# Performance work log

Measured on AMD Instinct MI355X. Metric: run time of the kernel, lower is better.

The kernel has to match this reference:

```python
import jax, jax.numpy as jnp
import numpy as np

N_BINS = 229
OUT_F = 88
MODEL = 128
W_SIZE = 30
WIN = 2 * W_SIZE + 1  # 61


def _window(spec):
    B, T, F = spec.shape
    padded = jnp.pad(spec, ((0, 0), (W_SIZE, W_SIZE), (0, 0)))
    idx = jnp.arange(T)[:, None] + jnp.arange(WIN)[None, :]
    return padded[:, idx, :]


def setup_inputs() -> dict:
    key = jax.random.key(0)
    ks = jax.random.split(key, 12)
    B, T = 4, 1024
    s = 0.05
    return {
        "spec": jax.random.normal(ks[0], (B, T, N_BINS), dtype=jnp.float32),
        # frame_stack: Linear(N_BINS -> OUT_F)
        "W_frame": jax.random.normal(ks[1], (N_BINS, OUT_F), dtype=jnp.float32) * s,
        "b_frame": jnp.zeros((OUT_F,), dtype=jnp.float32),
        # onset attention: Linear(N_BINS + N_BINS -> MODEL), v: Linear(MODEL -> 1, no bias)
        "W_attn_o": jax.random.normal(ks[2], (2 * N_BINS, MODEL), dtype=jnp.float32) * s,
        "b_attn_o": jnp.zeros((MODEL,), dtype=jnp.float32),
        "v_o": jax.random.normal(ks[3], (MODEL,), dtype=jnp.float32) * s,
        # onset linear1: Linear(N_BINS -> OUT_F)
        "W_lin1": jax.random.normal(ks[4], (N_BINS, OUT_F), dtype=jnp.float32) * s,
        "b_lin1": jnp.zeros((OUT_F,), dtype=jnp.float32),
        # combine attention: Linear(2*OUT_F + N_BINS -> MODEL)
        "W_attn_c": jax.random.normal(ks[5], (2 * OUT_F + N_BINS, MODEL), dtype=jnp.float32) * s,
        "b_attn_c": jnp.zeros((MODEL,), dtype=jnp.float32),
        "v_c": jax.random.normal(ks[6], (MODEL,), dtype=jnp.float32) * s,
        # combine linear: Linear(2*OUT_F + N_BINS -> OUT_F)
        "W_linc": jax.random.normal(ks[7], (2 * OUT_F + N_BINS, OUT_F), dtype=jnp.float32) * s,
        "b_linc": jnp.zeros((OUT_F,), dtype=jnp.float32),
    }


def _attend(hidden, win, Wa, ba, v):
    B, T, Wn, F = win.shape
    h = jnp.broadcast_to(hidden[:, :, None, :], (B, T, Wn, hidden.shape[-1]))
    energy = jnp.tanh(jnp.concatenate([h, win], axis=-1) @ Wa + ba)
    scores = energy @ v
    return jax.nn.softmax(scores, axis=-1)


def reference(spec, W_frame, b_frame, W_attn_o, b_attn_o, v_o, W_lin1, b_lin1,
              W_attn_c, b_attn_c, v_c, W_linc, b_linc):
    win = _window(spec)

    feat_pred = spec @ W_frame + b_frame  # [B,T,OUT_F]

    # Onset stack
    a_onset = _attend(spec, win, W_attn_o, b_attn_o, v_o)
    weighted_o = jnp.einsum('btw,btwf->btf', a_onset, win)  # [B,T,N_BINS]
    onset_pred = jax.nn.sigmoid(weighted_o @ W_lin1 + b_lin1)  # [B,T,OUT_F]

    # Combine stack
    x = jnp.concatenate([feat_pred, onset_pred], axis=-1)  # [B,T,2*OUT_F]
    a_frame = _attend(x, win, W_attn_c, b_attn_c, v_c)
    weighted_c = jnp.einsum('btw,btwf->btf', a_frame, win)  # [B,T,N_BINS]
    frame_pred = jax.nn.sigmoid(jnp.concatenate([x, weighted_c], axis=-1) @ W_linc + b_linc)

    return (frame_pred, a_frame[:, :, None, :], onset_pred, a_onset[:, :, None, :], feat_pred)
```

## Files before the change

kernel.cpp:

```cpp
#include <hip/hip_runtime.h>

#define NBINS 229
#define OUTF  88
#define MODEL 128
#define WSZ   30
#define WIN   61
#define TLEN  1024
#define BT    4096

#define NC1 648
#define NP1 704
#define NC2 216

typedef short bf16x8 __attribute__((ext_vector_type(8)));
typedef float f32x4 __attribute__((ext_vector_type(4)));
typedef unsigned short ushort_t;

__device__ __forceinline__ float sigmoid_f(float x) {
    return __builtin_amdgcn_rcpf(1.f + __expf(-x));
}
__device__ __forceinline__ ushort_t f2bf(float f) {
    unsigned u = __float_as_uint(f);
    return (ushort_t)((u + 0x7fffu + ((u >> 16) & 1u)) >> 16);
}

__device__ __forceinline__ float dot8(uint4 pv, float4 ha, float4 hb,
                                      float4 va, float4 vb) {
    float r;
    r  = va.x * __builtin_amdgcn_rcpf(__builtin_fmaf(ha.x, __uint_as_float(pv.x << 16), 1.f));
    r += va.y * __builtin_amdgcn_rcpf(__builtin_fmaf(ha.y, __uint_as_float(pv.x & 0xffff0000u), 1.f));
    r += va.z * __builtin_amdgcn_rcpf(__builtin_fmaf(ha.z, __uint_as_float(pv.y << 16), 1.f));
    r += va.w * __builtin_amdgcn_rcpf(__builtin_fmaf(ha.w, __uint_as_float(pv.y & 0xffff0000u), 1.f));
    r += vb.x * __builtin_amdgcn_rcpf(__builtin_fmaf(hb.x, __uint_as_float(pv.z << 16), 1.f));
    r += vb.y * __builtin_amdgcn_rcpf(__builtin_fmaf(hb.y, __uint_as_float(pv.z & 0xffff0000u), 1.f));
    r += vb.z * __builtin_amdgcn_rcpf(__builtin_fmaf(hb.z, __uint_as_float(pv.w << 16), 1.f));
    r += vb.w * __builtin_amdgcn_rcpf(__builtin_fmaf(hb.w, __uint_as_float(pv.w & 0xffff0000u), 1.f));
    return r;
}

__device__ __forceinline__ bf16x8 cvt8(f32x4 a, f32x4 b) {
    bf16x8 r;
    r[0] = (short)f2bf(a.x); r[1] = (short)f2bf(a.y);
    r[2] = (short)f2bf(a.z); r[3] = (short)f2bf(a.w);
    r[4] = (short)f2bf(b.x); r[5] = (short)f2bf(b.y);
    r[6] = (short)f2bf(b.z); r[7] = (short)f2bf(b.w);
    return r;
}
__device__ __forceinline__ bf16x8 loadA(const float* sp, int k0) {
    if (k0 > 228) return (bf16x8)(short)0;
    f32x4 a, b;
    __builtin_memcpy(&a, sp + k0, 16);
    if (k0 <= 216) {
        __builtin_memcpy(&b, sp + k0 + 4, 16);
    } else {
        b = (f32x4){sp[228], 0.f, 0.f, 0.f};
    }
    return cvt8(a, b);
}

#define GP_BLOCKS 897

__global__ __launch_bounds__(256) void gemm_prep(
    const float* __restrict__ spec,
    const float* __restrict__ Wf,  const float* __restrict__ bfr,
    const float* __restrict__ Wao, const float* __restrict__ bao,
    const float* __restrict__ Wl1,
    const float* __restrict__ Wac, const float* __restrict__ bac,
    const float* __restrict__ Wlc,
    const float* __restrict__ vo,  const float* __restrict__ vc,
    float* __restrict__ feat, float* __restrict__ EHo_,
    ushort_t* __restrict__ EPo_, ushort_t* __restrict__ EPc_,
    ushort_t* __restrict__ Rb_,  ushort_t* __restrict__ Qb_,
    ushort_t* __restrict__ B2b, float* __restrict__ bias2,
    float* __restrict__ sv)
{
    __shared__ ushort_t B1t[64 * 256];
    __shared__ float red[4];
    const int tid = threadIdx.x;
    const int b = blockIdx.x;

    if (b < 704) {
        const int e = b & 7, kf = b >> 3;
        const int rb = (e * 8 + (kf & 7)) * 64;
        const int cb = (kf >> 3) * 64;

        {
            const int n  = tid & 63;
            const int kq = tid >> 6;
            const int ng = cb + n;
            const float* srcp = nullptr; int sstr = 0;
            if (ng < 88)       { srcp = Wf  + ng;                          sstr = 88;  }
            else if (ng < 216) { srcp = Wao + (ng - 88);                   sstr = 128; }
            else if (ng < 344) { srcp = Wao + (size_t)NBINS * 128 + (ng - 216); sstr = 128; }
            else if (ng < 472) { srcp = Wac + (size_t)176 * 128 + (ng - 344);   sstr = 128; }
            else if (ng < 560) { srcp = Wl1 + (ng - 472);                  sstr = 88;  }
            else if (ng < NC1) { srcp = Wlc + (size_t)176 * 88 + (ng - 560);    sstr = 88; }
            const int n31 = n & 31;
#pragma unroll
            for (int it = 0; it < 8; it++) {
                const int k8 = kq * 8 + it * 32;
                bf16x8 vv;
#pragma unroll
                for (int j = 0; j < 8; j++) {
                    const int k = k8 + j;
                    float v = (srcp && k < NBINS) ? srcp[(size_t)k * sstr] : 0.f;
                    vv[j] = (short)f2bf(v);
                }
                const int chunk = (kq + 4 * it) ^ n31;
                *(bf16x8*)&B1t[n * 256 + chunk * 8] = vv;
            }
        }
        __syncthreads();

        const int wv = tid >> 6, ln = tid & 63;
        const int l15 = ln & 15, qd = ln >> 4;
        const float* sp = spec + (size_t)(rb + wv * 16 + l15) * NBINS;

        f32x4 acc[4];
#pragma unroll
        for (int nt = 0; nt < 4; nt++) acc[nt] = (f32x4){0.f, 0.f, 0.f, 0.f};

        bf16x8 af = loadA(sp, qd * 8);
#pragma unroll
        for (int it = 0; it < 8; it++) {
            const int nk = (it + 1 < 8) ? (it + 1) * 32 : 0;
            bf16x8 an = loadA(sp, nk + qd * 8);
            const int cq = qd + 4 * it;
#pragma unroll
            for (int nt = 0; nt < 4; nt++) {
                const int nn = nt * 16 + l15;
                bf16x8 bv = *(const bf16x8*)&B1t[nn * 256 + ((cq ^ (nn & 31)) << 3)];
                acc[nt] = __builtin_amdgcn_mfma_f32_16x16x32_bf16(
                    af, bv, acc[nt], 0, 0, 0);
            }
            af = an;
        }

        const int mbase = rb + wv * 16 + qd * 4;
#pragma unroll
        for (int nt = 0; nt < 4; nt++) {
            const int n = cb + nt * 16 + l15;
            if (n < NC1) {
                const float bn = (n < 88) ? bfr[n] : (n < 216 ? bao[n - 88] : 0.f);
#pragma unroll
                for (int r = 0; r < 4; r++) {
                    const int m = mbase + r;
                    float val = acc[nt][r] + bn;
                    if (n < 88) {
                        feat[(size_t)m * 88 + n] = val;
                    } else if (n < 216) {
                        EHo_[(size_t)m * 128 + (n - 88)] = __expf(val + val);
                    } else if (n < 344) {
                        EPo_[(size_t)m * 128 + (n - 216)] = f2bf(__expf(val + val));
                    } else if (n < 472) {
                        EPc_[(size_t)m * 128 + (n - 344)] = f2bf(__expf(val + val));
                    } else if (n < 560) {
                        Rb_[(size_t)m * 96 + (n - 472)] = f2bf(val);
                    } else {
                        Qb_[(size_t)m * 96 + (n - 560)] = f2bf(val);
                    }
                }
            }
        }
    } else if (b < 896) {
        int idx = (b - 704) * 256 + tid;
        int n = idx / 192, k = idx - n * 192;
        float v = 0.f;
        if (k < 176 && n < NC2)
            v = (n < 128) ? Wac[k * MODEL + n] : Wlc[k * 88 + (n - 128)];
        B2b[idx] = f2bf(v);
    } else {
        bias2[tid] = (tid < 128) ? bac[tid] : 0.f;
        int wid = tid >> 6, lane = tid & 63;
        const float* vp = (wid < 2) ? vo : vc;
        float val = vp[(wid & 1) * 64 + lane];
#pragma unroll
        for (int m = 32; m; m >>= 1) val += __shfl_xor(val, m, 64);
        if (lane == 0) red[wid] = val;
        __syncthreads();
        if (tid == 0) {
            sv[0] = red[0] + red[1];
            sv[1] = red[2] + red[3];
        }
    }
}

#define EPST 136
#define RST  96
#define XST  200

__global__ __launch_bounds__(512) void attn_fused(
    const float* __restrict__ EHo,
    const ushort_t* __restrict__ EPo_g,
    const ushort_t* __restrict__ Rb,
    const ushort_t* __restrict__ EPc_g,
    const ushort_t* __restrict__ Qb,
    const float* __restrict__ feat,
    const ushort_t* __restrict__ B2b,
    const float* __restrict__ bias2,
    const float* __restrict__ vo, const float* __restrict__ vc,
    const float* __restrict__ svp,
    const float* __restrict__ bl1, const float* __restrict__ blc,
    float* __restrict__ a_o_out, float* __restrict__ onset_out,
    float* __restrict__ a_c_out, float* __restrict__ frame_out)
{
    __shared__ alignas(16) ushort_t Plo[68 * EPST];
    __shared__ alignas(16) ushort_t Rl [68 * RST];
    __shared__ alignas(16) ushort_t Plc[68 * EPST];
    __shared__ alignas(16) ushort_t Ql [68 * RST];
    __shared__ alignas(16) ushort_t Xb [16 * XST];
    __shared__ alignas(16) float    EHc[8 * 128];
    __shared__ alignas(16) float    basec[8 * 88];

    const int tid = threadIdx.x;
    const int s0 = ((blockIdx.x & 7) * 64 + (blockIdx.x >> 3)) * 8;
    const int t0 = s0 & (TLEN - 1);

    for (int i = tid; i < 68 * 16; i += 512) {
        int j = i >> 4, c = (i & 15) * 8;
        int cs = ((i & 15) ^ ((j >> 3) & 7)) * 8;
        int tg = t0 + j - WSZ;
        uint4 vP = {0x3f803f80u, 0x3f803f80u, 0x3f803f80u, 0x3f803f80u};
        uint4 vC = vP;
        if ((unsigned)tg < (unsigned)TLEN) {
            vP = *(const uint4*)&EPo_g[(size_t)(s0 - WSZ + j) * 128 + c];
            vC = *(const uint4*)&EPc_g[(size_t)(s0 - WSZ + j) * 128 + c];
        }
        *(uint4*)&Plo[j * EPST + cs] = vP;
        *(uint4*)&Plc[j * EPST + cs] = vC;
    }
    for (int i = tid; i < 68 * 12; i += 512) {
        int j = i / 12, c = (i - j * 12) * 8;
        int tg = t0 + j - WSZ;
        uint4 vR = {0u, 0u, 0u, 0u}, vQ = {0u, 0u, 0u, 0u};
        if ((unsigned)tg < (unsigned)TLEN) {
            vR = *(const uint4*)&Rb[(size_t)(s0 - WSZ + j) * 96 + c];
            vQ = *(const uint4*)&Qb[(size_t)(s0 - WSZ + j) * 96 + c];
        }
        *(uint4*)&Rl[j * RST + c] = vR;
        *(uint4*)&Ql[j * RST + c] = vQ;
    }
    for (int i = tid; i < 16 * XST; i += 512) {
        int r = i / XST, k = i - r * XST;
        ushort_t v = 0;
        if (r < 8 && k < 88) v = f2bf(feat[(size_t)(s0 + r) * 88 + k]);
        Xb[i] = v;
    }
    __syncthreads();

    const int q = tid >> 6;
    const int w = tid & 63;
    const int s = s0 + q;
    const int su = __builtin_amdgcn_readfirstlane(s);
    const int row = q + ((w < WIN) ? w : 0);
    const int rsw = (row >> 3) & 7;

    {
        const ushort_t* pb = &Plo[row * EPST];
        const float* hrow = EHo + (size_t)su * 128;
        float accr = 0.f;
#pragma unroll
        for (int d8 = 0; d8 < 16; d8++) {
            uint4 pv = *(const uint4*)(pb + ((d8 ^ rsw) << 3));
            float4 ha = *(const float4*)(hrow + d8 * 8);
            float4 hb = *(const float4*)(hrow + d8 * 8 + 4);
            float4 va = *(const float4*)(vo + d8 * 8);
            float4 vb = *(const float4*)(vo + d8 * 8 + 4);
            accr += dot8(pv, ha, hb, va, vb);
        }
        float eng = svp[0] - 2.f * accr;
        float ex = (w < WIN) ? __expf(eng) : 0.f;
        float sm = ex;
#pragma unroll
        for (int m = 32; m; m >>= 1) sm += __shfl_xor(sm, m, 64);
        float a = ex * __builtin_amdgcn_rcpf(sm);
        if (w < WIN) a_o_out[(size_t)s * WIN + w] = a;

        if (w < 44) {
            const int f = 2 * w;
            float acc0 = bl1[f], acc1 = bl1[f + 1];
            const ushort_t* rr0 = &Rl[q * RST + f];
#pragma unroll
            for (int ww = 0; ww < WIN; ww++) {
                float aw = __uint_as_float(
                    __builtin_amdgcn_readlane(__float_as_uint(a), ww));
                unsigned u = *(const unsigned*)(rr0 + ww * RST);
                acc0 += aw * __uint_as_float(u << 16);
                acc1 += aw * __uint_as_float(u & 0xffff0000u);
            }
            float p0 = sigmoid_f(acc0), p1 = sigmoid_f(acc1);
            *(float2*)&onset_out[(size_t)s * OUTF + f] = make_float2(p0, p1);
            ushort2 o; o.x = f2bf(p0); o.y = f2bf(p1);
            *(ushort2*)&Xb[q * XST + 88 + f] = o;
        }
    }
    __syncthreads();

    {
        const int l15 = w & 15, qd = w >> 4;
#pragma unroll
        for (int rt = 0; rt < 2; rt++) {
            const int t = q + rt * 8;
            if (t < 14) {
                const int n0 = t * 16;
                const ushort_t* bp = B2b + (size_t)(n0 + l15) * 192 + qd * 8;
                const ushort_t* ap = &Xb[l15 * XST + qd * 8];
                f32x4 acc = (f32x4){0.f, 0.f, 0.f, 0.f};
#pragma unroll
                for (int it = 0; it < 6; it++) {
                    bf16x8 av = *(const bf16x8*)(ap + it * 32);
                    bf16x8 bv = *(const bf16x8*)(bp + it * 32);
                    acc = __builtin_amdgcn_mfma_f32_16x16x32_bf16(
                        av, bv, acc, 0, 0, 0);
                }
                if (qd < 2) {
                    const int n = n0 + l15;
                    const float b2 = bias2[n];
#pragma unroll
                    for (int r = 0; r < 4; r++) {
                        const int m = qd * 4 + r;
                        float val = acc[r] + b2;
                        if (n < 128)        EHc[m * 128 + n] = __expf(val + val);
                        else if (n < NC2)   basec[m * 88 + (n - 128)] = val;
                    }
                }
            }
        }
    }
    __syncthreads();

    {
        const ushort_t* pb = &Plc[row * EPST];
        const float* hl = &EHc[q * 128];
        float accr = 0.f;
#pragma unroll
        for (int d8 = 0; d8 < 16; d8++) {
            uint4 pv = *(const uint4*)(pb + ((d8 ^ rsw) << 3));
            float4 ha = *(const float4*)(hl + d8 * 8);
            float4 hb = *(const float4*)(hl + d8 * 8 + 4);
            float4 va = *(const float4*)(vc + d8 * 8);
            float4 vb = *(const float4*)(vc + d8 * 8 + 4);
            accr += dot8(pv, ha, hb, va, vb);
        }
        float eng = svp[1] - 2.f * accr;
        float ex = (w < WIN) ? __expf(eng) : 0.f;
        float sm = ex;
#pragma unroll
        for (int m = 32; m; m >>= 1) sm += __shfl_xor(sm, m, 64);
        float a = ex * __builtin_amdgcn_rcpf(sm);
        if (w < WIN) a_c_out[(size_t)s * WIN + w] = a;

        if (w < 44) {
            const int f = 2 * w;
            float acc0 = blc[f]     + basec[q * 88 + f];
            float acc1 = blc[f + 1] + basec[q * 88 + f + 1];
            const ushort_t* rr0 = &Ql[q * RST + f];
#pragma unroll
            for (int ww = 0; ww < WIN; ww++) {
                float aw = __uint_as_float(
                    __builtin_amdgcn_readlane(__float_as_uint(a), ww));
                unsigned u = *(const unsigned*)(rr0 + ww * RST);
                acc0 += aw * __uint_as_float(u << 16);
                acc1 += aw * __uint_as_float(u & 0xffff0000u);
            }
            float p0 = sigmoid_f(acc0), p1 = sigmoid_f(acc1);
            *(float2*)&frame_out[(size_t)s * OUTF + f] = make_float2(p0, p1);
        }
    }
}

extern "C" void kernel_launch(void* const* d_in, const int* in_sizes, int n_in,
                              void* d_out, int out_size, void* d_ws, size_t ws_size,
                              hipStream_t stream)
{
    const float* spec = (const float*)d_in[0];
    const float* Wf   = (const float*)d_in[1];
    const float* bf_  = (const float*)d_in[2];
    const float* Wao  = (const float*)d_in[3];
    const float* bao  = (const float*)d_in[4];
    const float* vo   = (const float*)d_in[5];
    const float* Wl1  = (const float*)d_in[6];
    const float* bl1  = (const float*)d_in[7];
    const float* Wac  = (const float*)d_in[8];
    const float* bac  = (const float*)d_in[9];
    const float* vc   = (const float*)d_in[10];
    const float* Wlc  = (const float*)d_in[11];
    const float* blc  = (const float*)d_in[12];

    float* out  = (float*)d_out;
    float* out0 = out;
    float* out1 = out + 360448;
    float* out2 = out + 610304;
    float* out3 = out + 970752;
    float* out4 = out + 1220608;

    float* ws = (float*)d_ws;
    float*    sv    = ws;
    float*    bias2 = ws + 16;
    ushort_t* B2b   = (ushort_t*)(ws + 272);
    float*    EHo   = ws + 24848;
    ushort_t* EPo   = (ushort_t*)(ws + 549136);
    ushort_t* EPc   = (ushort_t*)(ws + 811280);
    ushort_t* Rb    = (ushort_t*)(ws + 1073424);
    ushort_t* Qb    = (ushort_t*)(ws + 1270032);
    (void)ws_size; (void)in_sizes; (void)n_in; (void)out_size;

    gemm_prep<<<GP_BLOCKS, 256, 0, stream>>>(
        spec, Wf, bf_, Wao, bao, Wl1, Wac, bac, Wlc, vo, vc,
        out4, EHo, EPo, EPc, Rb, Qb, B2b, bias2, sv);

    attn_fused<<<BT / 8, 512, 0, stream>>>(
        EHo, EPo, Rb, EPc, Qb, out4, B2b, bias2, vo, vc, sv, bl1, blc,
        out3, out2, out1, out0);
}
```

Baseline: 115.8 us.

## Compute attention-weighted projections with banded MFMA instead of readlane FMA loops

The per-lane 61-step readlane/FMA loops that apply the attention weights to the projected window rows are replaced by a small matrix multiply on MFMA. The weights are written as bf16 into a banded shared-memory matrix (8 query rows by 96 padded window positions) and multiplied against the projected window rows, for both the onset and combine stacks. Shared memory is merged into one buffer so that K-padding rows past the window read neighbouring finite data, and pad columns are zeroed so those reads cannot inject NaNs. This adds two barriers and strided scalar LDS gathers for the B operand, and rounds the attention weights to bf16.

After: 111.9 us. 3.4% less time.

```diff
diff --git a/kernel.cpp b/kernel.cpp
--- a/kernel.cpp
+++ b/kernel.cpp
@@ -188,6 +188,17 @@
 #define EPST 136
 #define RST  96
 #define XST  200
+#define AST  104
+
+#define PLO_O 0
+#define RL_O  (68 * EPST)
+#define PLC_O (RL_O + 68 * RST)
+#define QL_O  (PLC_O + 68 * EPST)
+#define XB_O  (QL_O + 68 * RST)
+#define AM_O  (XB_O + 16 * XST)
+#define EHC_O (AM_O + 16 * AST)
+#define BSC_O (EHC_O + 2048)
+#define SH_U16 ((BSC_O + 1408))
 
 __global__ __launch_bounds__(512) void attn_fused(
     const float* __restrict__ EHo,
@@ -204,13 +215,15 @@
     float* __restrict__ a_o_out, float* __restrict__ onset_out,
     float* __restrict__ a_c_out, float* __restrict__ frame_out)
 {
-    __shared__ alignas(16) ushort_t Plo[68 * EPST];
-    __shared__ alignas(16) ushort_t Rl [68 * RST];
-    __shared__ alignas(16) ushort_t Plc[68 * EPST];
-    __shared__ alignas(16) ushort_t Ql [68 * RST];
-    __shared__ alignas(16) ushort_t Xb [16 * XST];
-    __shared__ alignas(16) float    EHc[8 * 128];
-    __shared__ alignas(16) float    basec[8 * 88];
+    __shared__ alignas(16) ushort_t SH[SH_U16];
+    ushort_t* Plo = SH + PLO_O;
+    ushort_t* Rl  = SH + RL_O;
+    ushort_t* Plc = SH + PLC_O;
+    ushort_t* Ql  = SH + QL_O;
+    ushort_t* Xb  = SH + XB_O;
+    ushort_t* Am  = SH + AM_O;
+    float*    EHc   = (float*)(SH + EHC_O);
+    float*    basec = (float*)(SH + BSC_O);
 
     const int tid = threadIdx.x;
     const int s0 = ((blockIdx.x & 7) * 64 + (blockIdx.x >> 3)) * 8;
@@ -229,6 +242,10 @@
         *(uint4*)&Plo[j * EPST + cs] = vP;
         *(uint4*)&Plc[j * EPST + cs] = vC;
     }
+    for (int i = tid; i < 68; i += 512) {
+        *(uint4*)&Plo[i * EPST + 128] = (uint4){0u, 0u, 0u, 0u};
+        *(uint4*)&Plc[i * EPST + 128] = (uint4){0u, 0u, 0u, 0u};
+    }
     for (int i = tid; i < 68 * 12; i += 512) {
         int j = i / 12, c = (i - j * 12) * 8;
         int tg = t0 + j - WSZ;
@@ -246,6 +263,11 @@
         if (r < 8 && k < 88) v = f2bf(feat[(size_t)(s0 + r) * 88 + k]);
         Xb[i] = v;
     }
+    {
+        unsigned* am32 = (unsigned*)Am;
+        for (int i = tid; i < 16 * 48; i += 512)
+            am32[(i / 48) * 52 + (i % 48)] = 0u;
+    }
     __syncthreads();
 
     const int q = tid >> 6;
@@ -254,6 +276,7 @@
     const int su = __builtin_amdgcn_readfirstlane(s);
     const int row = q + ((w < WIN) ? w : 0);
     const int rsw = (row >> 3) & 7;
+    const int l15 = w & 15, qd = w >> 4;
 
     {
         const ushort_t* pb = &Plo[row * EPST];
@@ -274,30 +297,39 @@
 #pragma unroll
         for (int m = 32; m; m >>= 1) sm += __shfl_xor(sm, m, 64);
         float a = ex * __builtin_amdgcn_rcpf(sm);
-        if (w < WIN) a_o_out[(size_t)s * WIN + w] = a;
-
-        if (w < 44) {
-            const int f = 2 * w;
-            float acc0 = bl1[f], acc1 = bl1[f + 1];
-            const ushort_t* rr0 = &Rl[q * RST + f];
-#pragma unroll
-            for (int ww = 0; ww < WIN; ww++) {
-                float aw = __uint_as_float(
-                    __builtin_amdgcn_readlane(__float_as_uint(a), ww));
-                unsigned u = *(const unsigned*)(rr0 + ww * RST);
-                acc0 += aw * __uint_as_float(u << 16);
-                acc1 += aw * __uint_as_float(u & 0xffff0000u);
-            }
-            float p0 = sigmoid_f(acc0), p1 = sigmoid_f(acc1);
-            *(float2*)&onset_out[(size_t)s * OUTF + f] = make_float2(p0, p1);
-            ushort2 o; o.x = f2bf(p0); o.y = f2bf(p1);
-            *(ushort2*)&Xb[q * XST + 88 + f] = o;
+        if (w < WIN) {
+            a_o_out[(size_t)s * WIN + w] = a;
+            Am[q * AST + q + w] = f2bf(a);
         }
     }
     __syncthreads();
 
+    if (q < 6) {
+        f32x4 acc = (f32x4){0.f, 0.f, 0.f, 0.f};
+#pragma unroll
+        for (int kk = 0; kk < 3; kk++) {
+            bf16x8 av = *(const bf16x8*)&Am[l15 * AST + kk * 32 + qd * 8];
+            bf16x8 bv;
+#pragma unroll
+            for (int j = 0; j < 8; j++)
+                bv[j] = (short)Rl[(kk * 32 + qd * 8 + j) * RST + q * 16 + l15];
+            acc = __builtin_amdgcn_mfma_f32_16x16x32_bf16(av, bv, acc, 0, 0, 0);
+        }
+        const int f = q * 16 + l15;
+        if (qd < 2 && f < 88) {
+            const float bb = bl1[f];
+#pragma unroll
+            for (int r = 0; r < 4; r++) {
+                const int m = qd * 4 + r;
+                float p = sigmoid_f(acc[r] + bb);
+                onset_out[(size_t)(s0 + m) * OUTF + f] = p;
+                Xb[m * XST + 88 + f] = f2bf(p);
+            }
+        }
+    }
+    __syncthreads();
+
     {
-        const int l15 = w & 15, qd = w >> 4;
 #pragma unroll
         for (int rt = 0; rt < 2; rt++) {
             const int t = q + rt * 8;
@@ -348,23 +380,33 @@
 #pragma unroll
         for (int m = 32; m; m >>= 1) sm += __shfl_xor(sm, m, 64);
         float a = ex * __builtin_amdgcn_rcpf(sm);
-        if (w < WIN) a_c_out[(size_t)s * WIN + w] = a;
-
-        if (w < 44) {
-            const int f = 2 * w;
-            float acc0 = blc[f]     + basec[q * 88 + f];
-            float acc1 = blc[f + 1] + basec[q * 88 + f + 1];
-            const ushort_t* rr0 = &Ql[q * RST + f];
-#pragma unroll
-            for (int ww = 0; ww < WIN; ww++) {
-                float aw = __uint_as_float(
-                    __builtin_amdgcn_readlane(__float_as_uint(a), ww));
-                unsigned u = *(const unsigned*)(rr0 + ww * RST);
-                acc0 += aw * __uint_as_float(u << 16);
-                acc1 += aw * __uint_as_float(u & 0xffff0000u);
-            }
-            float p0 = sigmoid_f(acc0), p1 = sigmoid_f(acc1);
-            *(float2*)&frame_out[(size_t)s * OUTF + f] = make_float2(p0, p1);
+        if (w < WIN) {
+            a_c_out[(size_t)s * WIN + w] = a;
+            Am[q * AST + q + w] = f2bf(a);
+        }
+    }
+    __syncthreads();
+
+    if (q < 6) {
+        f32x4 acc = (f32x4){0.f, 0.f, 0.f, 0.f};
+#pragma unroll
+        for (int kk = 0; kk < 3; kk++) {
+            bf16x8 av = *(const bf16x8*)&Am[l15 * AST + kk * 32 + qd * 8];
+            bf16x8 bv;
+#pragma unroll
+            for (int j = 0; j < 8; j++)
+                bv[j] = (short)Ql[(kk * 32 + qd * 8 + j) * RST + q * 16 + l15];
+            acc = __builtin_amdgcn_mfma_f32_16x16x32_bf16(av, bv, acc, 0, 0, 0);
+        }
+        const int f = q * 16 + l15;
+        if (qd < 2 && f < 88) {
+            const float bb = blc[f];
+#pragma unroll
+            for (int r = 0; r < 4; r++) {
+                const int m = qd * 4 + r;
+                float p = sigmoid_f(acc[r] + bb + basec[m * 88 + f]);
+                frame_out[(size_t)(s0 + m) * OUTF + f] = p;
+            }
         }
     }
 }
```
